# Optimization experiments

Hardware: AMD Instinct MI355X
Metric: run time of the kernel (lower is better)

The kernel has to match this reference:

```python
import jax, jax.numpy as jnp
import numpy as np

SCALES = (4, 2, 2)  # config.latent_structure.scaling_factors


def expand_length(x, scale):
    # Faithful to conv_transpose1d with an all-ones (D, D, scale) kernel at
    # stride=scale: out[b, l*scale + j, d] = sum_d' x[b, l, d'] for all j, d.
    # i.e. channel-sum broadcast to all channels, repeated `scale` times in L.
    s = jnp.sum(x, axis=-1, keepdims=True)            # [B, L, 1]
    y = jnp.broadcast_to(s, x.shape)                  # [B, L, D]
    return jnp.repeat(y, scale, axis=1)               # [B, L*scale, D]


def setup_inputs() -> dict:
    key = jax.random.key(0)
    k0, k1, k2, k3 = jax.random.split(key, 4)
    B, L, D0 = 8, 64, 256
    D1, D2, D3 = 512, 768, 768
    scale = 0.02
    return {
        "z_1": jax.random.normal(k0, (B, L, D0), jnp.float32),
        "W1": jax.random.normal(k1, (D0, D1), jnp.float32) * scale,
        "b1": jnp.zeros((D1,), jnp.float32),
        "W2": jax.random.normal(k2, (D1, D2), jnp.float32) * scale,
        "b2": jnp.zeros((D2,), jnp.float32),
        "W3": jax.random.normal(k3, (D2, D3), jnp.float32) * scale,
        "b3": jnp.zeros((D3,), jnp.float32),
    }


def reference(z_1, W1, b1, W2, b2, W3, b3):
    x = z_1
    for s in SCALES:                 # scaled_inputs is None -> plain loop
        x = expand_length(x, s)
    x = jnp.einsum("bld,de->ble", x, W1) + b1   # embedding_upscale1
    x = expand_length(x, SCALES[1])
    x = jnp.einsum("bld,de->ble", x, W2) + b2   # embedding_upscale2
    x = expand_length(x, SCALES[2])
    x = jnp.einsum("bld,de->ble", x, W3) + b3   # embedding_upscale3
    return x  # [8, 4096, 768]
```

## Files before the change

### kernel.cpp

```cpp
#include <hip/hip_runtime.h>

#define NF_W1P  0
#define NF_W2P  32
#define NF_B1   128
#define NF_B2   129
#define NF_S0   130
#define NF_CW3P 656
#define NF_CW3  6800
#define NF_U    7568

__device__ __forceinline__ float wave_reduce(float v) {
#pragma unroll
    for (int off = 32; off; off >>= 1) v += __shfl_down(v, off, 64);
    return v;
}

__device__ __forceinline__ float block_reduce_256(float v) {
    __shared__ float sm[4];
    v = wave_reduce(v);
    int lane = threadIdx.x & 63, wid = threadIdx.x >> 6;
    if (lane == 0) sm[wid] = v;
    __syncthreads();
    if (threadIdx.x == 0) v = sm[0] + sm[1] + sm[2] + sm[3];
    return v;
}

__global__ __launch_bounds__(256) void k_reduce(
    const float* __restrict__ z1, const float* __restrict__ W1,
    const float* __restrict__ b1, const float* __restrict__ W2,
    const float* __restrict__ b2, const float* __restrict__ W3,
    float* __restrict__ f) {
    const int blk = blockIdx.x, tid = threadIdx.x;
    if (blk < 128) {
        const float* p = (blk < 32) ? (W1 + blk * 4096) : (W2 + (blk - 32) * 4096);
        float s = 0.f;
#pragma unroll
        for (int i = 0; i < 16; ++i) s += p[tid + i * 256];
        s = block_reduce_256(s);
        if (tid == 0) f[blk] = s;
    } else if (blk == 128) {
        float s = b1[tid] + b1[tid + 256];
        s = block_reduce_256(s);
        if (tid == 0) f[NF_B1] = s;
    } else if (blk == 129) {
        float s = b2[tid] + b2[tid + 256] + b2[tid + 512];
        s = block_reduce_256(s);
        if (tid == 0) f[NF_B2] = s;
    } else if (blk < 258) {
        const int lane = tid & 63, wid = tid >> 6;
        const int row = (blk - 130) * 4 + wid;
        const float* p = z1 + row * 256;
        float s = p[lane] + p[lane + 64] + p[lane + 128] + p[lane + 192];
        s = wave_reduce(s);
        if (lane == 0) f[NF_S0 + row] = s;
    } else {
        const int g = blk - 258;
        const int cg = g % 3, rg = g / 3;
        const int e = cg * 256 + tid;
        const float* p = W3 + rg * 96 * 768 + e;
        float s = 0.f;
#pragma unroll 8
        for (int d = 0; d < 96; ++d) s += p[d * 768];
        f[NF_CW3P + rg * 768 + e] = s;
    }
}

__global__ __launch_bounds__(768) void k_combine(float* __restrict__ f) {
    const int tid = threadIdx.x;
    float c = 0.f;
#pragma unroll
    for (int r = 0; r < 8; ++r) c += f[NF_CW3P + r * 768 + tid];
    f[NF_CW3 + tid] = c;
    if (tid < 512) {
        float S1 = 0.f, S2 = 0.f;
        for (int i = 0; i < 32; ++i) S1 += f[NF_W1P + i];
        for (int i = 0; i < 96; ++i) S2 += f[NF_W2P + i];
        const float u = (65536.0f * f[NF_S0 + tid] * S1 + f[NF_B1]) * S2 + f[NF_B2];
        f[NF_U + tid] = u;
    }
}

__global__ __launch_bounds__(256) void k_write(
    const float* __restrict__ f, const float* __restrict__ b3,
    float* __restrict__ out) {
    const int tid = threadIdx.x;
    const int lane = tid & 63, wid = tid >> 6;
    const int row = blockIdx.x * 4 + wid;
    const float u = f[NF_U + (blockIdx.x >> 4)];
    const float4* __restrict__ cw4 = (const float4*)(f + NF_CW3);
    const float4* __restrict__ b4  = (const float4*)b3;
    float4* __restrict__ o = (float4*)(out + (size_t)row * 768);
#pragma unroll
    for (int k = 0; k < 3; ++k) {
        const int e4 = lane + k * 64;
        const float4 c = cw4[e4];
        const float4 b = b4[e4];
        float4 r;
        r.x = fmaf(u, c.x, b.x);
        r.y = fmaf(u, c.y, b.y);
        r.z = fmaf(u, c.z, b.z);
        r.w = fmaf(u, c.w, b.w);
        o[e4] = r;
    }
}

extern "C" void kernel_launch(void* const* d_in, const int* in_sizes, int n_in,
                              void* d_out, int out_size, void* d_ws, size_t ws_size,
                              hipStream_t stream) {
    const float* z1 = (const float*)d_in[0];
    const float* W1 = (const float*)d_in[1];
    const float* b1 = (const float*)d_in[2];
    const float* W2 = (const float*)d_in[3];
    const float* b2 = (const float*)d_in[4];
    const float* W3 = (const float*)d_in[5];
    const float* b3 = (const float*)d_in[6];
    float* out = (float*)d_out;
    float* f = (float*)d_ws;

    k_reduce<<<282, 256, 0, stream>>>(z1, W1, b1, W2, b2, W3, f);
    k_combine<<<1, 768, 0, stream>>>(f);
    k_write<<<8192, 256, 0, stream>>>(f, b3, out);
}
```

Before: 30.91 us.

## Fuse combine step into write kernel, write more rows per block, use nontemporal stores

Removes the single-block combine kernel. Each write block now sums the partial W3 column sums and the W1/W2 scalars itself and stages them in shared memory. Blocks drop from 8192 to 2048 and each writes 16 rows, using nontemporal stores for the roughly 100MB output. This saves one launch and a serial dependency, at the cost of every block redundantly reading about 24KB of partials from cache.

```diff
diff --git a/kernel.cpp b/kernel.cpp
--- a/kernel.cpp
+++ b/kernel.cpp
@@ -1,4 +1,6 @@
 #include <hip/hip_runtime.h>
+
+typedef float f4 __attribute__((ext_vector_type(4)));
 
 #define NF_W1P  0
 #define NF_W2P  32
@@ -6,8 +8,6 @@
 #define NF_B2   129
 #define NF_S0   130
 #define NF_CW3P 656
-#define NF_CW3  6800
-#define NF_U    7568
 
 __device__ __forceinline__ float wave_reduce(float v) {
 #pragma unroll
@@ -65,42 +65,58 @@
     }
 }
 
-__global__ __launch_bounds__(768) void k_combine(float* __restrict__ f) {
-    const int tid = threadIdx.x;
-    float c = 0.f;
-#pragma unroll
-    for (int r = 0; r < 8; ++r) c += f[NF_CW3P + r * 768 + tid];
-    f[NF_CW3 + tid] = c;
-    if (tid < 512) {
-        float S1 = 0.f, S2 = 0.f;
-        for (int i = 0; i < 32; ++i) S1 += f[NF_W1P + i];
-        for (int i = 0; i < 96; ++i) S2 += f[NF_W2P + i];
-        const float u = (65536.0f * f[NF_S0 + tid] * S1 + f[NF_B1]) * S2 + f[NF_B2];
-        f[NF_U + tid] = u;
-    }
-}
-
 __global__ __launch_bounds__(256) void k_write(
     const float* __restrict__ f, const float* __restrict__ b3,
     float* __restrict__ out) {
+    __shared__ float cw_sm[768];
+    __shared__ float b_sm[768];
+    __shared__ float u_sm;
     const int tid = threadIdx.x;
-    const int lane = tid & 63, wid = tid >> 6;
-    const int row = blockIdx.x * 4 + wid;
-    const float u = f[NF_U + (blockIdx.x >> 4)];
-    const float4* __restrict__ cw4 = (const float4*)(f + NF_CW3);
-    const float4* __restrict__ b4  = (const float4*)b3;
-    float4* __restrict__ o = (float4*)(out + (size_t)row * 768);
+
 #pragma unroll
     for (int k = 0; k < 3; ++k) {
-        const int e4 = lane + k * 64;
-        const float4 c = cw4[e4];
-        const float4 b = b4[e4];
-        float4 r;
-        r.x = fmaf(u, c.x, b.x);
-        r.y = fmaf(u, c.y, b.y);
-        r.z = fmaf(u, c.z, b.z);
-        r.w = fmaf(u, c.w, b.w);
-        o[e4] = r;
+        const int e = tid + k * 256;
+        float c = 0.f;
+#pragma unroll
+        for (int r = 0; r < 8; ++r) c += f[NF_CW3P + r * 768 + e];
+        cw_sm[e] = c;
+        b_sm[e] = b3[e];
+    }
+    if (tid < 64) {
+        float a = (tid < 32) ? f[NF_W1P + tid] : 0.f;
+        float b = f[NF_W2P + tid] + ((tid < 32) ? f[NF_W2P + 64 + tid] : 0.f);
+#pragma unroll
+        for (int off = 32; off; off >>= 1) {
+            a += __shfl_down(a, off, 64);
+            b += __shfl_down(b, off, 64);
+        }
+        if (tid == 0) {
+            const int uidx = blockIdx.x >> 2;
+            u_sm = (65536.0f * f[NF_S0 + uidx] * a + f[NF_B1]) * b + f[NF_B2];
+        }
+    }
+    __syncthreads();
+
+    const float u = u_sm;
+    const int lane = tid & 63, wid = tid >> 6;
+    const f4* __restrict__ cw4 = (const f4*)cw_sm;
+    const f4* __restrict__ b4  = (const f4*)b_sm;
+#pragma unroll
+    for (int r = 0; r < 4; ++r) {
+        const int row = blockIdx.x * 16 + wid * 4 + r;
+        f4* o = (f4*)(out + (size_t)row * 768);
+#pragma unroll
+        for (int k = 0; k < 3; ++k) {
+            const int e4 = lane + k * 64;
+            const f4 c = cw4[e4];
+            const f4 b = b4[e4];
+            f4 v;
+            v.x = fmaf(u, c.x, b.x);
+            v.y = fmaf(u, c.y, b.y);
+            v.z = fmaf(u, c.z, b.z);
+            v.w = fmaf(u, c.w, b.w);
+            __builtin_nontemporal_store(v, &o[e4]);
+        }
     }
 }
 
@@ -118,6 +134,5 @@
     float* f = (float*)d_ws;
 
     k_reduce<<<282, 256, 0, stream>>>(z1, W1, b1, W2, b2, W3, f);
-    k_combine<<<1, 768, 0, stream>>>(f);
-    k_write<<<8192, 256, 0, stream>>>(f, b3, out);
+    k_write<<<2048, 256, 0, stream>>>(f, b3, out);
 }
```

Measured after the change: 28.51 us. 1.08x faster.
